# Kernel tuning notes

Measured on AMD Instinct MI355X. Metric: run time of the kernel, lower is better.

Reference implementation:

```python
import jax, jax.numpy as jnp
import numpy as np

# irreps_in = irreps_out = 128x0e + 128x1o + 128x2e
MULS_IN = [128, 128, 128]
MULS_OUT = [128, 128, 128]
IR_DIMS = [1, 3, 5]          # dims of 0e, 1o, 2e
N = 100000                    # number of nodes / batch elements
IN_DIM = sum(m * d for m, d in zip(MULS_IN, IR_DIMS))    # 1152
OUT_DIM = sum(m * d for m, d in zip(MULS_OUT, IR_DIMS))  # 1152
W_NUMEL = sum(mi * mo for mi, mo in zip(MULS_IN, MULS_OUT))  # 49152


def setup_inputs() -> dict:
    key = jax.random.key(0)
    k1, k2 = jax.random.split(key)
    features = jax.random.normal(k1, (N, IN_DIM), dtype=jnp.float32)
    weight = jax.random.normal(k2, (W_NUMEL,), dtype=jnp.float32)
    return {"features": features, "weight": weight}


def reference(features, weight):
    # Faithful translation of e3nn o3.Linear forward with default (diagonal)
    # instructions and shared weights.
    size = features.shape[:-1]
    x = features.reshape(-1, IN_DIM)
    outs = []
    xoff = 0
    woff = 0
    for mu, mo, d in zip(MULS_IN, MULS_OUT, IR_DIMS):
        xi = x[:, xoff:xoff + mu * d].reshape(-1, mu, d)   # [z, u, i]
        w = weight[woff:woff + mu * mo].reshape(mu, mo)     # [u, w]
        # each output irrep has exactly 1 contributing instruction here
        alpha = 1.0 / np.sqrt(mu * 1.0)
        ein = jnp.einsum('uw,zui->zwi', w, xi) * jnp.asarray(alpha, xi.dtype)
        outs.append(ein.reshape(-1, mo * d))
        xoff += mu * d
        woff += mu * mo
    out = jnp.concatenate(outs, axis=1)
    return out.reshape(size + (OUT_DIM,))
```

## Files before the change

kernel.cpp:

```cpp
#include <hip/hip_runtime.h>
#include <hip/hip_bf16.h>


#define N_NODES 100000
#define IN_DIM  1152
#define ZT      32
#define NWG     (N_NODES / ZT)
#define THREADS 512

typedef __attribute__((ext_vector_type(8))) short bf16x8;
typedef __attribute__((ext_vector_type(4))) float f32x4;

__device__ __forceinline__ unsigned short f2bf(float x) {
    unsigned int u = __float_as_uint(x);
    unsigned int r = (u + 0x7FFFu + ((u >> 16) & 1u)) >> 16;
    return (unsigned short)r;
}

__global__ void prep_w_kernel(const float* __restrict__ w, unsigned int* __restrict__ wimg) {
    int t = blockIdx.x * 256 + threadIdx.x;
    if (t >= 3 * 8192) return;
    int b = t >> 13;
    int p = t & 8191;
    int A = p * 4;
    int row = A >> 8;
    int P = A ^ ((row & 7) << 4);
    int u0 = (P & 255) >> 1;
    const float alpha = 0.08838834764831845f;
    float v0 = w[b * 16384 + (u0    ) * 128 + row] * alpha;
    float v1 = w[b * 16384 + (u0 + 1) * 128 + row] * alpha;
    unsigned int pack = (unsigned int)f2bf(v0) | ((unsigned int)f2bf(v1) << 16);
    wimg[t] = pack;
}

template <int D>
__device__ __forceinline__ void run_block(const float* __restrict__ x,
                                          const unsigned int* __restrict__ wimg,
                                          float* __restrict__ out,
                                          char* smem, int tid, int zbase,
                                          int off, int wb) {
    __syncthreads();

    {
        const uint4* src = reinterpret_cast<const uint4*>(wimg) + wb * 2048;
        uint4* dst = reinterpret_cast<uint4*>(smem);
#pragma unroll
        for (int it = 0; it < 4; ++it)
            dst[it * THREADS + tid] = src[it * THREADS + tid];
    }

    {
        char* a_lds = smem + 32768;
        const float4* src4 = reinterpret_cast<const float4*>(x);
#pragma unroll
        for (int it = 0; it < 2 * D; ++it) {
            int e4 = it * THREADS + tid;
            int e = e4 * 4;
            int z = e / (128 * D);
            int rem = e - z * (128 * D);
            float4 v = src4[((zbase + z) * IN_DIM + off + rem) >> 2];
            if (D == 1) {
                int r = z;
                int byte = (r * 256 + rem * 2) ^ ((r & 7) << 4);
                unsigned int lo = (unsigned int)f2bf(v.x) | ((unsigned int)f2bf(v.y) << 16);
                unsigned int hi = (unsigned int)f2bf(v.z) | ((unsigned int)f2bf(v.w) << 16);
                uint2 pk; pk.x = lo; pk.y = hi;
                *reinterpret_cast<uint2*>(a_lds + byte) = pk;
            } else {
                float vv[4] = {v.x, v.y, v.z, v.w};
#pragma unroll
                for (int j = 0; j < 4; ++j) {
                    int rj = rem + j;
                    int u = rj / D;
                    int i = rj - u * D;
                    int r = i * 32 + z;
                    int byte = (r * 256 + u * 2) ^ ((r & 7) << 4);
                    *reinterpret_cast<unsigned short*>(a_lds + byte) = f2bf(vv[j]);
                }
            }
        }
    }
    __syncthreads();

    const int lane = tid & 63;
    const int wave = tid >> 6;
    const int n0 = wave * 16;
    const int lrow = lane & 15;
    const int lkb = (lane >> 4) * 16;
    constexpr int MT = 2 * D;
    f32x4 acc[MT];
#pragma unroll
    for (int m = 0; m < MT; ++m) acc[m] = (f32x4){0.f, 0.f, 0.f, 0.f};

    char* a_lds = smem + 32768;
#pragma unroll
    for (int ks = 0; ks < 4; ++ks) {
        int wrow = n0 + lrow;
        int wbyte = (wrow * 256 + ks * 64 + lkb) ^ ((wrow & 7) << 4);
        bf16x8 bfrag = *reinterpret_cast<bf16x8*>(smem + wbyte);
#pragma unroll
        for (int mt = 0; mt < MT; ++mt) {
            int ar = mt * 16 + lrow;
            int abyte = (ar * 256 + ks * 64 + lkb) ^ ((ar & 7) << 4);
            bf16x8 afrag = *reinterpret_cast<bf16x8*>(a_lds + abyte);
            acc[mt] = __builtin_amdgcn_mfma_f32_16x16x32_bf16(afrag, bfrag, acc[mt], 0, 0, 0);
        }
    }

    const int wcol = n0 + lrow;
#pragma unroll
    for (int mt = 0; mt < MT; ++mt) {
#pragma unroll
        for (int j = 0; j < 4; ++j) {
            int r = mt * 16 + (lane >> 4) * 4 + j;
            int z = r & 31;
            int i = r >> 5;
            out[(zbase + z) * IN_DIM + off + wcol * D + i] = acc[mt][j];
        }
    }
}

__global__ __launch_bounds__(THREADS, 4)
void linear_e3nn_kernel(const float* __restrict__ x,
                        const unsigned int* __restrict__ wimg,
                        float* __restrict__ out) {
    __shared__ __align__(16) char smem[32768 + 40960];
    const int tid = threadIdx.x;
    const int zbase = blockIdx.x * ZT;
    run_block<1>(x, wimg, out, smem, tid, zbase, 0,   0);
    run_block<3>(x, wimg, out, smem, tid, zbase, 128, 1);
    run_block<5>(x, wimg, out, smem, tid, zbase, 512, 2);
}

extern "C" void kernel_launch(void* const* d_in, const int* in_sizes, int n_in,
                              void* d_out, int out_size, void* d_ws, size_t ws_size,
                              hipStream_t stream) {
    const float* features = (const float*)d_in[0];
    const float* weight   = (const float*)d_in[1];
    float* out = (float*)d_out;
    unsigned int* wimg = (unsigned int*)d_ws;

    prep_w_kernel<<<96, 256, 0, stream>>>(weight, wimg);
    linear_e3nn_kernel<<<NWG, THREADS, 0, stream>>>(features, wimg, out);
}
```

Measured before the change: 781.2 us.

## Prefetch feature tiles into registers, double-buffer LDS, load weights directly into fragments

Rebuilds the per-block flow so the global loads for later irrep blocks are issued early into registers, overlapping their latency with the staging and MFMA work of earlier blocks, with two LDS buffers in alternation. The weight prep kernel now writes weights already in per-lane MFMA fragment order, so each wave loads its B fragments straight from global memory rather than copying the weight image to LDS. This raises register pressure (up to 18 float4 of prefetch plus weight fragments) and LDS use grows to 80KB per block, which may limit occupancy.

```diff
diff --git a/kernel.cpp b/kernel.cpp
--- a/kernel.cpp
+++ b/kernel.cpp
@@ -17,73 +17,87 @@
     return (unsigned short)r;
 }
 
-__global__ void prep_w_kernel(const float* __restrict__ w, unsigned int* __restrict__ wimg) {
+__global__ void prep_w_kernel(const float* __restrict__ w, uint4* __restrict__ wimg) {
     int t = blockIdx.x * 256 + threadIdx.x;
-    if (t >= 3 * 8192) return;
-    int b = t >> 13;
-    int p = t & 8191;
-    int A = p * 4;
-    int row = A >> 8;
-    int P = A ^ ((row & 7) << 4);
-    int u0 = (P & 255) >> 1;
+    if (t >= 6144) return;
+    int b   = t >> 11;
+    int r   = t & 2047;
+    int wv  = r >> 8;
+    int r2  = r & 255;
+    int ks  = r2 >> 6;
+    int l   = r2 & 63;
+    int wrow = wv * 16 + (l & 15);
+    int u0   = ks * 32 + (l >> 4) * 8;
     const float alpha = 0.08838834764831845f;
-    float v0 = w[b * 16384 + (u0    ) * 128 + row] * alpha;
-    float v1 = w[b * 16384 + (u0 + 1) * 128 + row] * alpha;
-    unsigned int pack = (unsigned int)f2bf(v0) | ((unsigned int)f2bf(v1) << 16);
-    wimg[t] = pack;
+    unsigned int pk[4];
+#pragma unroll
+    for (int j2 = 0; j2 < 4; ++j2) {
+        float v0 = w[b * 16384 + (u0 + 2 * j2    ) * 128 + wrow] * alpha;
+        float v1 = w[b * 16384 + (u0 + 2 * j2 + 1) * 128 + wrow] * alpha;
+        pk[j2] = (unsigned int)f2bf(v0) | ((unsigned int)f2bf(v1) << 16);
+    }
+    uint4 o; o.x = pk[0]; o.y = pk[1]; o.z = pk[2]; o.w = pk[3];
+    wimg[t] = o;
 }
 
 template <int D>
-__device__ __forceinline__ void run_block(const float* __restrict__ x,
-                                          const unsigned int* __restrict__ wimg,
-                                          float* __restrict__ out,
-                                          char* smem, int tid, int zbase,
-                                          int off, int wb) {
-    __syncthreads();
+__device__ __forceinline__ void issue_loads(const float* __restrict__ x, int tid,
+                                            int zbase, int off, float4 (&p)[2 * D]) {
+    const float4* src4 = reinterpret_cast<const float4*>(x);
+#pragma unroll
+    for (int it = 0; it < 2 * D; ++it) {
+        int e4 = it * THREADS + tid;
+        int e = e4 * 4;
+        int z = e / (128 * D);
+        int rem = e - z * (128 * D);
+        p[it] = src4[((zbase + z) * IN_DIM + off + rem) >> 2];
+    }
+}
 
-    {
-        const uint4* src = reinterpret_cast<const uint4*>(wimg) + wb * 2048;
-        uint4* dst = reinterpret_cast<uint4*>(smem);
+template <int D>
+__device__ __forceinline__ void stage_tile(char* a_lds, int tid, const float4 (&p)[2 * D]) {
 #pragma unroll
-        for (int it = 0; it < 4; ++it)
-            dst[it * THREADS + tid] = src[it * THREADS + tid];
-    }
-
-    {
-        char* a_lds = smem + 32768;
-        const float4* src4 = reinterpret_cast<const float4*>(x);
+    for (int it = 0; it < 2 * D; ++it) {
+        int e4 = it * THREADS + tid;
+        int e = e4 * 4;
+        int z = e / (128 * D);
+        int rem = e - z * (128 * D);
+        float4 v = p[it];
+        if (D == 1) {
+            int r = z;
+            int byte = (r * 256 + rem * 2) ^ ((r & 7) << 4);
+            unsigned int lo = (unsigned int)f2bf(v.x) | ((unsigned int)f2bf(v.y) << 16);
+            unsigned int hi = (unsigned int)f2bf(v.z) | ((unsigned int)f2bf(v.w) << 16);
+            uint2 pk; pk.x = lo; pk.y = hi;
+            *reinterpret_cast<uint2*>(a_lds + byte) = pk;
+        } else {
+            float vv[4] = {v.x, v.y, v.z, v.w};
 #pragma unroll
-        for (int it = 0; it < 2 * D; ++it) {
-            int e4 = it * THREADS + tid;
-            int e = e4 * 4;
-            int z = e / (128 * D);
-            int rem = e - z * (128 * D);
-            float4 v = src4[((zbase + z) * IN_DIM + off + rem) >> 2];
-            if (D == 1) {
-                int r = z;
-                int byte = (r * 256 + rem * 2) ^ ((r & 7) << 4);
-                unsigned int lo = (unsigned int)f2bf(v.x) | ((unsigned int)f2bf(v.y) << 16);
-                unsigned int hi = (unsigned int)f2bf(v.z) | ((unsigned int)f2bf(v.w) << 16);
-                uint2 pk; pk.x = lo; pk.y = hi;
-                *reinterpret_cast<uint2*>(a_lds + byte) = pk;
-            } else {
-                float vv[4] = {v.x, v.y, v.z, v.w};
-#pragma unroll
-                for (int j = 0; j < 4; ++j) {
-                    int rj = rem + j;
-                    int u = rj / D;
-                    int i = rj - u * D;
-                    int r = i * 32 + z;
-                    int byte = (r * 256 + u * 2) ^ ((r & 7) << 4);
-                    *reinterpret_cast<unsigned short*>(a_lds + byte) = f2bf(vv[j]);
-                }
+            for (int j = 0; j < 4; ++j) {
+                int rj = rem + j;
+                int u = rj / D;
+                int i = rj - u * D;
+                int r = i * 32 + z;
+                int byte = (r * 256 + u * 2) ^ ((r & 7) << 4);
+                *reinterpret_cast<unsigned short*>(a_lds + byte) = f2bf(vv[j]);
             }
         }
     }
-    __syncthreads();
+}
 
-    const int lane = tid & 63;
-    const int wave = tid >> 6;
+__device__ __forceinline__ void load_w(const uint4* __restrict__ wimg, int b,
+                                       int wave, int lane, bf16x8 (&wf)[4]) {
+#pragma unroll
+    for (int ks = 0; ks < 4; ++ks) {
+        uint4 u = wimg[((b * 8 + wave) * 4 + ks) * 64 + lane];
+        wf[ks] = *reinterpret_cast<bf16x8*>(&u);
+    }
+}
+
+template <int D>
+__device__ __forceinline__ void compute_store(const char* a_lds, const bf16x8 (&wf)[4],
+                                              float* __restrict__ out, int zbase,
+                                              int off, int lane, int wave) {
     const int n0 = wave * 16;
     const int lrow = lane & 15;
     const int lkb = (lane >> 4) * 16;
@@ -92,18 +106,14 @@
 #pragma unroll
     for (int m = 0; m < MT; ++m) acc[m] = (f32x4){0.f, 0.f, 0.f, 0.f};
 
-    char* a_lds = smem + 32768;
 #pragma unroll
     for (int ks = 0; ks < 4; ++ks) {
-        int wrow = n0 + lrow;
-        int wbyte = (wrow * 256 + ks * 64 + lkb) ^ ((wrow & 7) << 4);
-        bf16x8 bfrag = *reinterpret_cast<bf16x8*>(smem + wbyte);
 #pragma unroll
         for (int mt = 0; mt < MT; ++mt) {
             int ar = mt * 16 + lrow;
             int abyte = (ar * 256 + ks * 64 + lkb) ^ ((ar & 7) << 4);
-            bf16x8 afrag = *reinterpret_cast<bf16x8*>(a_lds + abyte);
-            acc[mt] = __builtin_amdgcn_mfma_f32_16x16x32_bf16(afrag, bfrag, acc[mt], 0, 0, 0);
+            bf16x8 afrag = *reinterpret_cast<const bf16x8*>(a_lds + abyte);
+            acc[mt] = __builtin_amdgcn_mfma_f32_16x16x32_bf16(afrag, wf[ks], acc[mt], 0, 0, 0);
         }
     }
 
@@ -122,14 +132,35 @@
 
 __global__ __launch_bounds__(THREADS, 4)
 void linear_e3nn_kernel(const float* __restrict__ x,
-                        const unsigned int* __restrict__ wimg,
+                        const uint4* __restrict__ wimg,
                         float* __restrict__ out) {
-    __shared__ __align__(16) char smem[32768 + 40960];
+    __shared__ __align__(16) char smem[2 * 40960];
+    char* buf0 = smem;
+    char* buf1 = smem + 40960;
     const int tid = threadIdx.x;
+    const int lane = tid & 63;
+    const int wave = tid >> 6;
     const int zbase = blockIdx.x * ZT;
-    run_block<1>(x, wimg, out, smem, tid, zbase, 0,   0);
-    run_block<3>(x, wimg, out, smem, tid, zbase, 128, 1);
-    run_block<5>(x, wimg, out, smem, tid, zbase, 512, 2);
+
+    float4 p0[2];  issue_loads<1>(x, tid, zbase, 0,   p0);
+    float4 p1[6];  issue_loads<3>(x, tid, zbase, 128, p1);
+    bf16x8 w0[4];  load_w(wimg, 0, wave, lane, w0);
+
+    stage_tile<1>(buf0, tid, p0);
+    __syncthreads();
+
+    float4 p2[10]; issue_loads<5>(x, tid, zbase, 512, p2);
+    bf16x8 w1[4];  load_w(wimg, 1, wave, lane, w1);
+    compute_store<1>(buf0, w0, out, zbase, 0, lane, wave);
+    stage_tile<3>(buf1, tid, p1);
+    __syncthreads();
+
+    bf16x8 w2[4];  load_w(wimg, 2, wave, lane, w2);
+    compute_store<3>(buf1, w1, out, zbase, 128, lane, wave);
+    stage_tile<5>(buf0, tid, p2);
+    __syncthreads();
+
+    compute_store<5>(buf0, w2, out, zbase, 512, lane, wave);
 }
 
 extern "C" void kernel_launch(void* const* d_in, const int* in_sizes, int n_in,
@@ -138,8 +169,8 @@
     const float* features = (const float*)d_in[0];
     const float* weight   = (const float*)d_in[1];
     float* out = (float*)d_out;
-    unsigned int* wimg = (unsigned int*)d_ws;
+    uint4* wimg = (uint4*)d_ws;
 
-    prep_w_kernel<<<96, 256, 0, stream>>>(weight, wimg);
+    prep_w_kernel<<<24, 256, 0, stream>>>(weight, wimg);
     linear_e3nn_kernel<<<NWG, THREADS, 0, stream>>>(features, wimg, out);
 }
```

Result: no change. 779.0 us (-0.3%).
